# Optimization experiments

Hardware: AMD Instinct MI355X
Metric: run time of the kernel (lower is better)

Reference implementation:

```python
import jax, jax.numpy as jnp
import numpy as np

NUM_HEADS = 12


def setup_inputs() -> dict:
    key = jax.random.key(0)
    ks = jax.random.split(key, 5)
    B, S, D = 4, 2048, 768
    scale = 0.02
    return {
        "hidden_states": jax.random.normal(ks[0], (B, S, D), dtype=jnp.float32),
        "c_attn_w": jax.random.normal(ks[1], (D, 3 * D), dtype=jnp.float32) * scale,
        "c_attn_b": jax.random.normal(ks[2], (3 * D,), dtype=jnp.float32) * scale,
        "c_proj_w": jax.random.normal(ks[3], (D, D), dtype=jnp.float32) * scale,
        "c_proj_b": jax.random.normal(ks[4], (D,), dtype=jnp.float32) * scale,
    }


def reference(hidden_states, c_attn_w, c_attn_b, c_proj_w, c_proj_b):
    B, S, D = hidden_states.shape
    H = NUM_HEADS
    hd = D // H

    # fused QKV projection (HF Conv1D: x @ W + b, W is [in, out])
    qkv = hidden_states @ c_attn_w + c_attn_b  # [B, S, 3D]
    q, k, v = jnp.split(qkv, 3, axis=-1)

    def split_heads(t):
        return t.reshape(B, S, H, hd).transpose(0, 2, 1, 3)  # [B, H, S, hd]

    q, k, v = split_heads(q), split_heads(k), split_heads(v)

    # scaled dot-product scores (scale_attn_weights=True -> / sqrt(head_dim))
    scores = jnp.einsum("bhqd,bhkd->bhqk", q, k) / jnp.asarray(
        np.sqrt(hd), dtype=q.dtype
    )

    # causal mask: where(tril, scores, dtype_min) as in eager GPT2Attention
    causal = jnp.tril(jnp.ones((S, S), dtype=bool))
    mask_value = jnp.finfo(scores.dtype).min
    scores = jnp.where(causal[None, None, :, :], scores, mask_value)

    attn = jax.nn.softmax(scores, axis=-1)  # attn_dropout p=0 (eval)

    out = jnp.einsum("bhqk,bhkd->bhqd", attn, v)
    out = out.transpose(0, 2, 1, 3).reshape(B, S, D)  # merge heads

    # output projection (resid_dropout p=0)
    return out @ c_proj_w + c_proj_b
```

## Files before the change

kernel.cpp:

```cpp
#include <hip/hip_runtime.h>
#include <stdint.h>

typedef __attribute__((ext_vector_type(8))) short short8;
typedef __attribute__((ext_vector_type(4))) short short4v;
typedef __attribute__((ext_vector_type(8))) __bf16 bf16x8;
typedef __attribute__((ext_vector_type(4))) float f32x4;

#define SEQ 2048
#define DMODEL 768
#define NHEAD 12
#define HD 64
#define NBATCH 4

#define QSCALE 0.18033688011112042f

__device__ __forceinline__ float bf2f(unsigned short u) {
    return __uint_as_float(((unsigned int)u) << 16);
}
__device__ __forceinline__ unsigned short f2bf(float f) {
    unsigned int u = __float_as_uint(f);
    u += 0x7fffu + ((u >> 16) & 1u);
    return (unsigned short)(u >> 16);
}
__device__ __forceinline__ unsigned short f2bfn(float f) {
    union { __bf16 h; unsigned short u; } cv;
    cv.h = (__bf16)f;
    return cv.u;
}
__device__ __forceinline__ short8 cvt8(float4 a, float4 b) {
    short8 r;
    r[0] = (short)f2bf(a.x); r[1] = (short)f2bf(a.y);
    r[2] = (short)f2bf(a.z); r[3] = (short)f2bf(a.w);
    r[4] = (short)f2bf(b.x); r[5] = (short)f2bf(b.y);
    r[6] = (short)f2bf(b.z); r[7] = (short)f2bf(b.w);
    return r;
}
__device__ __forceinline__ f32x4 mfma16(short8 a, short8 b, f32x4 c) {
    return __builtin_amdgcn_mfma_f32_16x16x32_bf16(
        __builtin_bit_cast(bf16x8, a), __builtin_bit_cast(bf16x8, b), c, 0, 0, 0);
}
__device__ __forceinline__ f32x4 mfma16k16(short4v a, short4v b, f32x4 c) {
#if __has_builtin(__builtin_amdgcn_mfma_f32_16x16x16bf16_1k)
    return __builtin_amdgcn_mfma_f32_16x16x16bf16_1k(a, b, c, 0, 0, 0);
#else
    asm("v_mfma_f32_16x16x16_bf16 %0, %1, %2, %0" : "+v"(c) : "v"(a), "v"(b));
    return c;
#endif
}
__device__ __forceinline__ void gload16(const unsigned short* g, unsigned short* l) {
    __builtin_amdgcn_global_load_lds(
        (const __attribute__((address_space(1))) unsigned int*)g,
        (__attribute__((address_space(3))) unsigned int*)l, 16, 0, 0);
}

__global__ void detect_k(const unsigned short* x, const unsigned short* w1,
                         const unsigned short* b1, const unsigned short* w2,
                         const unsigned short* b2, int* flags) {
    const int w = threadIdx.x >> 6, l = threadIdx.x & 63;
    if (w >= 5) return;
    const unsigned short* ptrs[5] = {x, w1, b1, w2, b2};
    const unsigned short* p = ptrs[w];
    float mx = 0.f;
    for (int j = l; j < 1024; j += 64) {
        float v = fabsf(bf2f(p[j]));
        if (!(v <= 1e30f)) v = 1e31f;
        if (v > mx) mx = v;
    }
#pragma unroll
    for (int off = 1; off < 64; off <<= 1) mx = fmaxf(mx, __shfl_xor(mx, off, 64));
    if (l == 0) flags[w] = (mx > 1e3f) ? 1 : 0;
}

__global__ __launch_bounds__(256) void cvt_x(
    const float* __restrict__ Xf, const unsigned short* __restrict__ Xh,
    unsigned short* __restrict__ Xb, const int* __restrict__ flags, int n8) {
    int i = blockIdx.x * 256 + threadIdx.x;
    if (i >= n8) return;
    if (flags[0]) {
        float4 a = ((const float4*)Xf)[(size_t)i * 2];
        float4 b = ((const float4*)Xf)[(size_t)i * 2 + 1];
        *(short8*)&Xb[(size_t)i * 8] = cvt8(a, b);
    } else {
        ((uint4*)Xb)[i] = ((const uint4*)Xh)[i];
    }
}

__device__ __forceinline__ void wt_body(
    unsigned short (*tile)[65], const float* __restrict__ Wf,
    const unsigned short* __restrict__ Wh, unsigned short* __restrict__ Wt,
    int R, int C, bool f32, int bx, int by, int t) {

    const int c0 = bx * 64, r0 = by * 64;
    const int ri = t >> 2, cj = (t & 3) * 16;

    if (f32) {
#pragma unroll
        for (int u = 0; u < 4; u++) {
            float4 v = *(const float4*)&Wf[(size_t)(r0 + ri) * C + c0 + cj + u * 4];
            tile[ri][cj + u * 4 + 0] = f2bf(v.x);
            tile[ri][cj + u * 4 + 1] = f2bf(v.y);
            tile[ri][cj + u * 4 + 2] = f2bf(v.z);
            tile[ri][cj + u * 4 + 3] = f2bf(v.w);
        }
    } else {
        uint4 a = *(const uint4*)&Wh[(size_t)(r0 + ri) * C + c0 + cj];
        uint4 b = *(const uint4*)&Wh[(size_t)(r0 + ri) * C + c0 + cj + 8];
        *(uint4*)&tile[ri][cj] = a;
        *(uint4*)&tile[ri][cj + 8] = b;
    }
    __syncthreads();

    const int ci = t >> 2, rj = (t & 3) * 16;
    unsigned short tmp[16];
#pragma unroll
    for (int u = 0; u < 16; u++) tmp[u] = tile[rj + u][ci];
    *(uint4*)&Wt[(size_t)(c0 + ci) * R + r0 + rj]     = *(uint4*)&tmp[0];
    *(uint4*)&Wt[(size_t)(c0 + ci) * R + r0 + rj + 8] = *(uint4*)&tmp[8];
}

__global__ __launch_bounds__(256) void convert_wt_both(
    const float* __restrict__ Wf1, const unsigned short* __restrict__ Wh1,
    unsigned short* __restrict__ Wt1,
    const float* __restrict__ Wf2, const unsigned short* __restrict__ Wh2,
    unsigned short* __restrict__ Wt2, const int* __restrict__ flags) {

    __shared__ unsigned short tile[64][65];
    const int t = threadIdx.x;
    if (blockIdx.y < 12) {
        wt_body(tile, Wf1, Wh1, Wt1, 768, 2304, flags[1] != 0,
                (int)blockIdx.x, (int)blockIdx.y, t);
    } else {
        if (blockIdx.x >= 12) return;
        wt_body(tile, Wf2, Wh2, Wt2, 768, 768, flags[3] != 0,
                (int)blockIdx.x, (int)blockIdx.y - 12, t);
    }
}

#define GSTG(buf, s) do {                                                          \
    unsigned short* BsF_ = &Bs[buf][0][0];                                         \
    gload16(&Bp[(size_t)(ch0 >> 2) * K + (s) * 32 + (ch0 & 3) * 8],                \
            BsF_ + (size_t)(w * 2 + 0) * 512);                                     \
    gload16(&Bp[(size_t)(ch1 >> 2) * K + (s) * 32 + (ch1 & 3) * 8],                \
            BsF_ + (size_t)(w * 2 + 1) * 512);                                     \
    if (af32) {                                                                    \
        float4 f0_ = *(const float4*)&Afp[(size_t)arow * K + (s) * 32 + acol];     \
        float4 f1_ = *(const float4*)&Afp[(size_t)arow * K + (s) * 32 + acol + 4]; \
        float4 f2_ = *(const float4*)&Afp[(size_t)(arow + 64) * K + (s) * 32 + acol];     \
        float4 f3_ = *(const float4*)&Afp[(size_t)(arow + 64) * K + (s) * 32 + acol + 4]; \
        *(short8*)&As[buf][arow][acol]      = cvt8(f0_, f1_);                      \
        *(short8*)&As[buf][arow + 64][acol] = cvt8(f2_, f3_);                      \
    } else {                                                                       \
        unsigned short* AsF_ = &As[buf][0][0];                                     \
        gload16(&Ahp[(size_t)(ch0 >> 2) * K + (s) * 32 + (ch0 & 3) * 8],           \
                AsF_ + (size_t)(w * 2 + 0) * 512);                                 \
        gload16(&Ahp[(size_t)(ch1 >> 2) * K + (s) * 32 + (ch1 & 3) * 8],           \
                AsF_ + (size_t)(w * 2 + 1) * 512);                                 \
    }                                                                              \
} while (0)

#define GSYNC() do {                                                               \
    if (af32) asm volatile("s_waitcnt vmcnt(0) lgkmcnt(0)" ::: "memory");          \
    else      asm volatile("s_waitcnt vmcnt(0)" ::: "memory");                     \
    __builtin_amdgcn_s_barrier();                                                  \
} while (0)

__global__ __launch_bounds__(256, 4) void gemm_bt(
    const float* __restrict__ Af, const unsigned short* __restrict__ Ah,
    const unsigned short* __restrict__ Bt,
    const float* __restrict__ biasf, const unsigned short* __restrict__ biash,
    int K, int mode, const int* __restrict__ flags, int aFidx, int bFidx,
    unsigned short* __restrict__ out0, unsigned short* __restrict__ out1,
    unsigned short* __restrict__ out2, float* __restrict__ outf) {

    __shared__ __align__(16) unsigned short As[2][128][32];
    __shared__ __align__(16) unsigned short Bs[2][128][32];

    int bx = blockIdx.x, by = blockIdx.y;
    {
        const int nwg = (int)(gridDim.x * gridDim.y);
        if ((nwg & 7) == 0) {
            int bid = by * gridDim.x + bx;
            const int cpx = nwg >> 3;
            bid = (bid & 7) * cpx + (bid >> 3);
            bx = bid % gridDim.x;
            by = bid / gridDim.x;
        }
    }
    const int mBase = by * 128;
    const int nBase = bx * 128;
    const int t = threadIdx.x;
    const int w = t >> 6, l = t & 63, lr = l & 15, lk = l >> 4;
    const int wr = w >> 1, wc = w & 1;

    const bool af32 = (aFidx >= 0) && (flags[aFidx] != 0);
    const bool bf32 = flags[bFidx] != 0;

    f32x4 zero = {0.f, 0.f, 0.f, 0.f};
    f32x4 acc[4][4];
#pragma unroll
    for (int i = 0; i < 4; i++)
#pragma unroll
        for (int j = 0; j < 4; j++) acc[i][j] = zero;

    const int arow = t >> 2;
    const int acol = (t & 3) * 8;
    const float* Afp = Af + (size_t)mBase * K;
    const unsigned short* Ahp = Ah + (size_t)mBase * K;
    const unsigned short* Bp = Bt + (size_t)nBase * K;

    const int ch0 = (w * 2 + 0) * 64 + l;
    const int ch1 = (w * 2 + 1) * 64 + l;

    const int nsteps = K >> 5;

    GSTG(0, 0);
    GSYNC();

    int cur = 0;
    for (int s = 0; s < nsteps; ++s) {
        if (s + 1 < nsteps) GSTG(cur ^ 1, s + 1);

        short8 a[4], b[4];
#pragma unroll
        for (int i = 0; i < 4; i++)
            a[i] = *(const short8*)&As[cur][wr * 64 + i * 16 + lr][lk * 8];
#pragma unroll
        for (int j = 0; j < 4; j++)
            b[j] = *(const short8*)&Bs[cur][wc * 64 + j * 16 + lr][lk * 8];
#pragma unroll
        for (int i = 0; i < 4; i++)
#pragma unroll
            for (int j = 0; j < 4; j++) acc[i][j] = mfma16(a[i], b[j], acc[i][j]);

        if (s + 1 < nsteps) GSYNC();
        cur ^= 1;
    }

#pragma unroll
    for (int j = 0; j < 4; j++) {
        int col = nBase + wc * 64 + j * 16 + lr;
        float bv = bf32 ? biasf[col] : bf2f(biash[col]);
        if (mode == 0 && col >= 1536) {
            int c2 = col - 1536;
            int h = c2 >> 6, d = c2 & 63;
#pragma unroll
            for (int i = 0; i < 4; i++) {
                int row0 = mBase + wr * 64 + i * 16 + lk * 4;
                int bb = row0 >> 11, s0 = row0 & 2047;
                short4v hv4;
#pragma unroll
                for (int r = 0; r < 4; r++) hv4[r] = (short)f2bf(acc[i][j][r] + bv);
                *(short4v*)&out2[(((size_t)(bb * NHEAD + h)) * HD + d) * SEQ + s0] = hv4;
            }
        } else {
#pragma unroll
            for (int i = 0; i < 4; i++) {
                int row0 = mBase + wr * 64 + i * 16 + lk * 4;
#pragma unroll
                for (int r = 0; r < 4; r++) {
                    int row = row0 + r;
                    float fv = acc[i][j][r] + bv;
                    if (mode == 0) {
                        int bb = row >> 11;
                        int s  = row & 2047;
                        if (col < 768) {
                            int h = col >> 6, d = col & 63;
                            out0[(((size_t)(bb * NHEAD + h)) * SEQ + s) * HD + d] =
                                f2bf(fv * QSCALE);
                        } else {
                            int c2 = col - 768;
                            int h = c2 >> 6, d = c2 & 63;
                            out1[(((size_t)(bb * NHEAD + h)) * SEQ + s) * HD + d] =
                                f2bf(fv);
                        }
                    } else {
                        outf[(size_t)row * DMODEL + col] = fv;
                    }
                }
            }
        }
    }
}

#define STAGE(buf, tile) do {                                                  \
    _Pragma("unroll")                                                          \
    for (int q_ = 0; q_ < 2; ++q_) {                                           \
        const int c_ = w * 128 + q_ * 64 + l;                                  \
        const int row_ = c_ >> 3;                                              \
        const int ch_ = (c_ & 7) ^ (row_ & 7);                                 \
        gload16(&Kp[(size_t)((tile) * 64 + row_) * HD + ch_ * 8],              \
                &Ks[buf][(w * 128 + q_ * 64) * 8]);                            \
        gload16(&Vp[(size_t)row_ * SEQ + (tile) * 64 + ch_ * 8],               \
                &Vs[buf][(w * 128 + q_ * 64) * 8]);                            \
    }                                                                          \
} while (0)

__global__ __launch_bounds__(256, 3) void flash_attn(
    const unsigned short* __restrict__ Q, const unsigned short* __restrict__ Km,
    const unsigned short* __restrict__ Vt, unsigned short* __restrict__ Oatt) {

    const int h  = blockIdx.x;
    const int px = (7 * blockIdx.y + blockIdx.x + blockIdx.z) & 15;
    const int b  = blockIdx.z;
    const int bh = b * NHEAD + h;
    const int qtA = 31 - px;
    const int qtB = px;
    const int t = threadIdx.x, w = t >> 6, l = t & 63, lr = l & 15, lk = l >> 4;
    const int qbA = qtA * 64 + w * 16;
    const int qbB = qtB * 64 + w * 16;

    const unsigned short* Qp = Q + (size_t)bh * SEQ * HD;
    const unsigned short* Kp = Km + (size_t)bh * SEQ * HD;
    const unsigned short* Vp = Vt + (size_t)bh * HD * SEQ;

    __shared__ __align__(16) unsigned short Ks[3][4096];
    __shared__ __align__(16) unsigned short Vs[3][4096];

    short8 qA0 = *(const short8*)&Qp[(size_t)(qbA + lr) * HD + lk * 8];
    short8 qA1 = *(const short8*)&Qp[(size_t)(qbA + lr) * HD + 32 + lk * 8];
    short8 qB0 = *(const short8*)&Qp[(size_t)(qbB + lr) * HD + lk * 8];
    short8 qB1 = *(const short8*)&Qp[(size_t)(qbB + lr) * HD + 32 + lk * 8];

    f32x4 zero = {0.f, 0.f, 0.f, 0.f};
    f32x4 oA[4], oB[4];
    float lsumA = 0.f, lsumB = 0.f;
#pragma unroll
    for (int dt = 0; dt < 4; dt++) { oA[dt] = zero; oB[dt] = zero; }

    STAGE(0, 0);
    STAGE(1, 1);
    asm volatile("s_waitcnt vmcnt(4)" ::: "memory");
    __builtin_amdgcn_s_barrier();

    int cur = 0;
    for (int kt = 0; kt <= qtA; ++kt) {
        const bool pf = (kt + 2 <= qtA);
        if (pf) {
            const int st = (cur == 0) ? 2 : cur - 1;
            STAGE(st, kt + 2);
        }
        const bool doB = (kt <= qtB);

        f32x4 s0[4], s1[4];
        __builtin_amdgcn_s_setprio(1);
#pragma unroll
        for (int ct = 0; ct < 4; ct++) {
            const int row = ct * 16 + lr, sw = row & 7;
            short8 k0 = *(const short8*)&Ks[cur][(row * 8 + (lk ^ sw)) * 8];
            short8 k1 = *(const short8*)&Ks[cur][(row * 8 + ((4 | lk) ^ sw)) * 8];
            s0[ct] = mfma16(k0, qA0, zero);
            s0[ct] = mfma16(k1, qA1, s0[ct]);
            if (doB) {
                s1[ct] = mfma16(k0, qB0, zero);
                s1[ct] = mfma16(k1, qB1, s1[ct]);
            }
        }
        __builtin_amdgcn_s_setprio(0);

        short4v vf[4][4];
#pragma unroll
        for (int dt = 0; dt < 4; dt++) {
            const int row = dt * 16 + lr;
            const int sw = row & 7;
#pragma unroll
            for (int ct = 0; ct < 4; ct++) {
                const int g = 2 * ct + (lk >> 1);
                const int hh = lk & 1;
                vf[dt][ct] = *(const short4v*)&Vs[cur][(row * 8 + (g ^ sw)) * 8 + hh * 4];
            }
        }

        short4v paA[4];
        {
            float p[4][4];
#pragma unroll
            for (int ct = 0; ct < 4; ct++)
#pragma unroll
                for (int r = 0; r < 4; r++) p[ct][r] = exp2f(s0[ct][r]);
            if (kt == qtA) {
                const int qrow = qbA + lr;
#pragma unroll
                for (int ct = 0; ct < 4; ct++)
#pragma unroll
                    for (int r = 0; r < 4; r++) {
                        const int key = kt * 64 + ct * 16 + lk * 4 + r;
                        if (key > qrow) p[ct][r] = 0.0f;
                    }
            }
#pragma unroll
            for (int ct = 0; ct < 4; ct++)
                lsumA += (p[ct][0] + p[ct][1]) + (p[ct][2] + p[ct][3]);
#pragma unroll
            for (int ct = 0; ct < 4; ct++) {
                short4v pk;
#pragma unroll
                for (int r = 0; r < 4; r++) pk[r] = (short)f2bfn(p[ct][r]);
                paA[ct] = pk;
            }
        }
        __builtin_amdgcn_s_setprio(1);
#pragma unroll
        for (int dt = 0; dt < 4; dt++)
#pragma unroll
            for (int ct = 0; ct < 4; ct++)
                oA[dt] = mfma16k16(paA[ct], vf[dt][ct], oA[dt]);
        __builtin_amdgcn_s_setprio(0);

        if (doB) {
            short4v paB[4];
            float p[4][4];
#pragma unroll
            for (int ct = 0; ct < 4; ct++)
#pragma unroll
                for (int r = 0; r < 4; r++) p[ct][r] = exp2f(s1[ct][r]);
            if (kt == qtB) {
                const int qrow = qbB + lr;
#pragma unroll
                for (int ct = 0; ct < 4; ct++)
#pragma unroll
                    for (int r = 0; r < 4; r++) {
                        const int key = kt * 64 + ct * 16 + lk * 4 + r;
                        if (key > qrow) p[ct][r] = 0.0f;
                    }
            }
#pragma unroll
            for (int ct = 0; ct < 4; ct++)
                lsumB += (p[ct][0] + p[ct][1]) + (p[ct][2] + p[ct][3]);
#pragma unroll
            for (int ct = 0; ct < 4; ct++) {
                short4v pk;
#pragma unroll
                for (int r = 0; r < 4; r++) pk[r] = (short)f2bfn(p[ct][r]);
                paB[ct] = pk;
            }
            __builtin_amdgcn_s_setprio(1);
#pragma unroll
            for (int dt = 0; dt < 4; dt++)
#pragma unroll
                for (int ct = 0; ct < 4; ct++)
                    oB[dt] = mfma16k16(paB[ct], vf[dt][ct], oB[dt]);
            __builtin_amdgcn_s_setprio(0);
        }

        if (kt < qtA) {
            if (pf) asm volatile("s_waitcnt vmcnt(4)" ::: "memory");
            else    asm volatile("s_waitcnt vmcnt(0)" ::: "memory");
            __builtin_amdgcn_s_barrier();
        }
        cur = (cur == 2) ? 0 : cur + 1;
    }

    lsumA += __shfl_xor(lsumA, 16, 64);
    lsumA += __shfl_xor(lsumA, 32, 64);
    lsumB += __shfl_xor(lsumB, 16, 64);
    lsumB += __shfl_xor(lsumB, 32, 64);

#pragma unroll
    for (int r = 0; r < 4; r++) {
        const float invA = 1.0f / __shfl(lsumA, lk * 4 + r, 64);
        const float invB = 1.0f / __shfl(lsumB, lk * 4 + r, 64);
        const int rowA = qbA + lk * 4 + r;
        const int rowB = qbB + lk * 4 + r;
#pragma unroll
        for (int dt = 0; dt < 4; dt++) {
            Oatt[((size_t)(b * SEQ) + rowA) * DMODEL + h * HD + dt * 16 + lr] =
                f2bfn(oA[dt][r] * invA);
            Oatt[((size_t)(b * SEQ) + rowB) * DMODEL + h * HD + dt * 16 + lr] =
                f2bfn(oB[dt][r] * invB);
        }
    }
}

extern "C" void kernel_launch(void* const* d_in, const int* in_sizes, int n_in,
                              void* d_out, int out_size, void* d_ws, size_t ws_size,
                              hipStream_t stream) {
    const void *X = d_in[0], *W1 = d_in[1], *b1 = d_in[2], *W2 = d_in[3], *b2 = d_in[4];
    for (int i = 0; i < n_in; i++) {
        switch (in_sizes[i]) {
            case NBATCH * SEQ * DMODEL: X  = d_in[i]; break;
            case DMODEL * 3 * DMODEL:   W1 = d_in[i]; break;
            case 3 * DMODEL:            b1 = d_in[i]; break;
            case DMODEL * DMODEL:       W2 = d_in[i]; break;
            case DMODEL:                b2 = d_in[i]; break;
        }
    }
    float* out = (float*)d_out;

    int* flags = (int*)d_ws;
    unsigned short* base = (unsigned short*)d_ws + 64;
    unsigned short* Wt1 = base;
    unsigned short* Wt2 = Wt1 + (size_t)2304 * 768;

    const size_t headElems = (size_t)NHEAD * SEQ * HD;
    const size_t xElems = (size_t)NBATCH * SEQ * DMODEL;
    const size_t fixedElems = 64 + (size_t)2304 * 768 + (size_t)768 * 768;
    const size_t mergedNeed = (fixedElems + xElems + 4 * NBATCH * headElems) * 2 + 1024;
    const bool merged = ws_size >= mergedNeed;

    detect_k<<<1, 320, 0, stream>>>(
        (const unsigned short*)X, (const unsigned short*)W1,
        (const unsigned short*)b1, (const unsigned short*)W2,
        (const unsigned short*)b2, flags);

    convert_wt_both<<<dim3(36, 24), 256, 0, stream>>>(
        (const float*)W1, (const unsigned short*)W1, Wt1,
        (const float*)W2, (const unsigned short*)W2, Wt2, flags);

    if (merged) {
        unsigned short* Xb  = Wt2 + (size_t)768 * 768;
        unsigned short* Qw  = Xb + xElems;
        unsigned short* Kw  = Qw + (size_t)NBATCH * headElems;
        unsigned short* Vtw = Kw + (size_t)NBATCH * headElems;
        unsigned short* Aw  = Vtw + (size_t)NBATCH * headElems;

        cvt_x<<<(int)((xElems / 8 + 255) / 256), 256, 0, stream>>>(
            (const float*)X, (const unsigned short*)X, Xb, flags, (int)(xElems / 8));

        gemm_bt<<<dim3(2304 / 128, NBATCH * SEQ / 128), 256, 0, stream>>>(
            nullptr, Xb, Wt1,
            (const float*)b1, (const unsigned short*)b1,
            DMODEL, 0, flags, -1, 2, Qw, Kw, Vtw, nullptr);

        flash_attn<<<dim3(NHEAD, 16, NBATCH), 256, 0, stream>>>(Qw, Kw, Vtw, Aw);

        gemm_bt<<<dim3(768 / 128, NBATCH * SEQ / 128), 256, 0, stream>>>(
            nullptr, Aw, Wt2,
            (const float*)b2, (const unsigned short*)b2,
            DMODEL, 1, flags, -1, 4, nullptr, nullptr, nullptr, out);
    } else {
        unsigned short* Qw  = Wt2 + (size_t)768 * 768;
        unsigned short* Kw  = Qw + headElems;
        unsigned short* Vtw = Kw + headElems;
        unsigned short* Aw  = Vtw + headElems;
        for (int batch = 0; batch < NBATCH; ++batch) {
            const size_t xoff = (size_t)batch * SEQ * DMODEL;

            gemm_bt<<<dim3(2304 / 128, SEQ / 128), 256, 0, stream>>>(
                (const float*)X + xoff, (const unsigned short*)X + xoff, Wt1,
                (const float*)b1, (const unsigned short*)b1,
                DMODEL, 0, flags, 0, 2, Qw, Kw, Vtw, nullptr);

            flash_attn<<<dim3(NHEAD, 16, 1), 256, 0, stream>>>(Qw, Kw, Vtw, Aw);

            gemm_bt<<<dim3(768 / 128, SEQ / 128), 256, 0, stream>>>(
                nullptr, Aw, Wt2,
                (const float*)b2, (const unsigned short*)b2,
                DMODEL, 1, flags, -1, 4, nullptr, nullptr, nullptr, out + xoff);
        }
    }
}
```

Baseline: 236.8 us.

## Triple-buffer GEMM staging and unroll attention loop by three with constant buffer offsets

The GEMM kernel moves from double to triple buffered LDS tiles, prefetching two steps ahead with a partial vmcnt wait instead of draining all loads. Its launch-bounds occupancy hint drops from 4 to 3 to fit the larger shared memory. The flash attention loop is unrolled three times so the rotating buffer index becomes a compile-time constant, and the swizzled LDS offsets are precomputed outside the loop. This aims to hide global load latency and remove per-iteration address math, at the cost of more LDS, lower occupancy in the GEMM and larger code.

Result: slower. 305.9 us (+29.2%).

```diff
diff --git a/kernel.cpp b/kernel.cpp
--- a/kernel.cpp
+++ b/kernel.cpp
@@ -158,13 +158,7 @@
     }                                                                              \
 } while (0)
 
-#define GSYNC() do {                                                               \
-    if (af32) asm volatile("s_waitcnt vmcnt(0) lgkmcnt(0)" ::: "memory");          \
-    else      asm volatile("s_waitcnt vmcnt(0)" ::: "memory");                     \
-    __builtin_amdgcn_s_barrier();                                                  \
-} while (0)
-
-__global__ __launch_bounds__(256, 4) void gemm_bt(
+__global__ __launch_bounds__(256, 3) void gemm_bt(
     const float* __restrict__ Af, const unsigned short* __restrict__ Ah,
     const unsigned short* __restrict__ Bt,
     const float* __restrict__ biasf, const unsigned short* __restrict__ biash,
@@ -172,8 +166,8 @@
     unsigned short* __restrict__ out0, unsigned short* __restrict__ out1,
     unsigned short* __restrict__ out2, float* __restrict__ outf) {
 
-    __shared__ __align__(16) unsigned short As[2][128][32];
-    __shared__ __align__(16) unsigned short Bs[2][128][32];
+    __shared__ __align__(16) unsigned short As[3][128][32];
+    __shared__ __align__(16) unsigned short Bs[3][128][32];
 
     int bx = blockIdx.x, by = blockIdx.y;
     {
@@ -214,11 +208,18 @@
     const int nsteps = K >> 5;
 
     GSTG(0, 0);
-    GSYNC();
+    GSTG(1, 1);
+    if (af32) { asm volatile("s_waitcnt vmcnt(0) lgkmcnt(0)" ::: "memory"); }
+    else      { asm volatile("s_waitcnt vmcnt(4)" ::: "memory"); }
+    __builtin_amdgcn_s_barrier();
 
     int cur = 0;
     for (int s = 0; s < nsteps; ++s) {
-        if (s + 1 < nsteps) GSTG(cur ^ 1, s + 1);
+        const bool pf = (s + 2 < nsteps);
+        if (pf) {
+            const int st = (cur == 0) ? 2 : cur - 1;
+            GSTG(st, s + 2);
+        }
 
         short8 a[4], b[4];
 #pragma unroll
@@ -232,8 +233,13 @@
 #pragma unroll
             for (int j = 0; j < 4; j++) acc[i][j] = mfma16(a[i], b[j], acc[i][j]);
 
-        if (s + 1 < nsteps) GSYNC();
-        cur ^= 1;
+        if (s + 1 < nsteps) {
+            if (af32)    { asm volatile("s_waitcnt vmcnt(0) lgkmcnt(0)" ::: "memory"); }
+            else if (pf) { asm volatile("s_waitcnt vmcnt(4)" ::: "memory"); }
+            else         { asm volatile("s_waitcnt vmcnt(0)" ::: "memory"); }
+            __builtin_amdgcn_s_barrier();
+        }
+        cur = (cur == 2) ? 0 : cur + 1;
     }
 
 #pragma unroll
@@ -295,6 +301,113 @@
     }                                                                          \
 } while (0)
 
+#define FBODY(CUR) do {                                                        \
+    const bool pf = (kt + 2 <= qtA);                                           \
+    if (pf) STAGE((((CUR) + 2) % 3), kt + 2);                                  \
+    const bool doB = (kt <= qtB);                                              \
+    f32x4 s0[4], s1[4];                                                        \
+    __builtin_amdgcn_s_setprio(1);                                             \
+    _Pragma("unroll")                                                          \
+    for (int ct = 0; ct < 4; ct++) {                                           \
+        short8 k0 = *(const short8*)&KsF[(CUR) * 4096 + ct * 1024 + k0off];    \
+        short8 k1 = *(const short8*)&KsF[(CUR) * 4096 + ct * 1024 + k1off];    \
+        s0[ct] = mfma16(k0, qA0, zero);                                        \
+        s0[ct] = mfma16(k1, qA1, s0[ct]);                                      \
+        if (doB) {                                                             \
+            s1[ct] = mfma16(k0, qB0, zero);                                    \
+            s1[ct] = mfma16(k1, qB1, s1[ct]);                                  \
+        }                                                                      \
+    }                                                                          \
+    __builtin_amdgcn_s_setprio(0);                                             \
+    short4v vf0[4], vf1[4], vf2[4], vf3[4];                                    \
+    _Pragma("unroll")                                                          \
+    for (int dt = 0; dt < 4; dt++) {                                           \
+        vf0[dt] = *(const short4v*)&VsF[(CUR) * 4096 + dt * 1024 + voff0];     \
+        vf1[dt] = *(const short4v*)&VsF[(CUR) * 4096 + dt * 1024 + voff1];     \
+        vf2[dt] = *(const short4v*)&VsF[(CUR) * 4096 + dt * 1024 + voff2];     \
+        vf3[dt] = *(const short4v*)&VsF[(CUR) * 4096 + dt * 1024 + voff3];     \
+    }                                                                          \
+    short4v paA[4];                                                            \
+    {                                                                          \
+        float p[4][4];                                                         \
+        _Pragma("unroll")                                                      \
+        for (int ct = 0; ct < 4; ct++)                                         \
+            _Pragma("unroll")                                                  \
+            for (int r = 0; r < 4; r++) p[ct][r] = exp2f(s0[ct][r]);           \
+        if (kt == qtA) {                                                       \
+            const int qrow = qbA + lr;                                         \
+            _Pragma("unroll")                                                  \
+            for (int ct = 0; ct < 4; ct++)                                     \
+                _Pragma("unroll")                                              \
+                for (int r = 0; r < 4; r++) {                                  \
+                    const int key = kt * 64 + ct * 16 + lk * 4 + r;            \
+                    if (key > qrow) p[ct][r] = 0.0f;                           \
+                }                                                              \
+        }                                                                      \
+        _Pragma("unroll")                                                      \
+        for (int ct = 0; ct < 4; ct++)                                         \
+            lsumA += (p[ct][0] + p[ct][1]) + (p[ct][2] + p[ct][3]);            \
+        _Pragma("unroll")                                                      \
+        for (int ct = 0; ct < 4; ct++) {                                       \
+            short4v pk;                                                        \
+            _Pragma("unroll")                                                  \
+            for (int r = 0; r < 4; r++) pk[r] = (short)f2bfn(p[ct][r]);        \
+            paA[ct] = pk;                                                      \
+        }                                                                      \
+    }                                                                          \
+    __builtin_amdgcn_s_setprio(1);                                             \
+    _Pragma("unroll")                                                          \
+    for (int dt = 0; dt < 4; dt++) {                                           \
+        oA[dt] = mfma16k16(paA[0], vf0[dt], oA[dt]);                           \
+        oA[dt] = mfma16k16(paA[1], vf1[dt], oA[dt]);                           \
+        oA[dt] = mfma16k16(paA[2], vf2[dt], oA[dt]);                           \
+        oA[dt] = mfma16k16(paA[3], vf3[dt], oA[dt]);                           \
+    }                                                                          \
+    __builtin_amdgcn_s_setprio(0);                                             \
+    if (doB) {                                                                 \
+        short4v paB[4];                                                        \
+        float p[4][4];                                                         \
+        _Pragma("unroll")                                                      \
+        for (int ct = 0; ct < 4; ct++)                                         \
+            _Pragma("unroll")                                                  \
+            for (int r = 0; r < 4; r++) p[ct][r] = exp2f(s1[ct][r]);           \
+        if (kt == qtB) {                                                       \
+            const int qrow = qbB + lr;                                         \
+            _Pragma("unroll")                                                  \
+            for (int ct = 0; ct < 4; ct++)                                     \
+                _Pragma("unroll")                                              \
+                for (int r = 0; r < 4; r++) {                                  \
+                    const int key = kt * 64 + ct * 16 + lk * 4 + r;            \
+                    if (key > qrow) p[ct][r] = 0.0f;                           \
+                }                                                              \
+        }                                                                      \
+        _Pragma("unroll")                                                      \
+        for (int ct = 0; ct < 4; ct++)                                         \
+            lsumB += (p[ct][0] + p[ct][1]) + (p[ct][2] + p[ct][3]);            \
+        _Pragma("unroll")                                                      \
+        for (int ct = 0; ct < 4; ct++) {                                       \
+            short4v pk;                                                        \
+            _Pragma("unroll")                                                  \
+            for (int r = 0; r < 4; r++) pk[r] = (short)f2bfn(p[ct][r]);        \
+            paB[ct] = pk;                                                      \
+        }                                                                      \
+        __builtin_amdgcn_s_setprio(1);                                         \
+        _Pragma("unroll")                                                      \
+        for (int dt = 0; dt < 4; dt++) {                                       \
+            oB[dt] = mfma16k16(paB[0], vf0[dt], oB[dt]);                       \
+            oB[dt] = mfma16k16(paB[1], vf1[dt], oB[dt]);                       \
+            oB[dt] = mfma16k16(paB[2], vf2[dt], oB[dt]);                       \
+            oB[dt] = mfma16k16(paB[3], vf3[dt], oB[dt]);                       \
+        }                                                                      \
+        __builtin_amdgcn_s_setprio(0);                                         \
+    }                                                                          \
+    if (kt < qtA) {                                                            \
+        if (pf) asm volatile("s_waitcnt vmcnt(4)" ::: "memory");               \
+        else    asm volatile("s_waitcnt vmcnt(0)" ::: "memory");               \
+        __builtin_amdgcn_s_barrier();                                          \
+    }                                                                          \
+} while (0)
+
 __global__ __launch_bounds__(256, 3) void flash_attn(
     const unsigned short* __restrict__ Q, const unsigned short* __restrict__ Km,
     const unsigned short* __restrict__ Vt, unsigned short* __restrict__ Oatt) {
@@ -315,6 +428,8 @@
 
     __shared__ __align__(16) unsigned short Ks[3][4096];
     __shared__ __align__(16) unsigned short Vs[3][4096];
+    const unsigned short* KsF = &Ks[0][0];
+    const unsigned short* VsF = &Vs[0][0];
 
     short8 qA0 = *(const short8*)&Qp[(size_t)(qbA + lr) * HD + lk * 8];
     short8 qA1 = *(const short8*)&Qp[(size_t)(qbA + lr) * HD + 32 + lk * 8];
@@ -327,128 +442,29 @@
 #pragma unroll
     for (int dt = 0; dt < 4; dt++) { oA[dt] = zero; oB[dt] = zero; }
 
+    const int sw = lr & 7;
+    const int k0off = lr * 64 + ((lk ^ sw) * 8);
+    const int k1off = lr * 64 + ((((4 | lk)) ^ sw) * 8);
+    const int q2 = lk >> 1, hh2 = (lk & 1) * 4;
+    const int voff0 = lr * 64 + (((0 + q2) ^ sw) * 8) + hh2;
+    const int voff1 = lr * 64 + (((2 + q2) ^ sw) * 8) + hh2;
+    const int voff2 = lr * 64 + (((4 + q2) ^ sw) * 8) + hh2;
+    const int voff3 = lr * 64 + (((6 + q2) ^ sw) * 8) + hh2;
+
     STAGE(0, 0);
     STAGE(1, 1);
     asm volatile("s_waitcnt vmcnt(4)" ::: "memory");
     __builtin_amdgcn_s_barrier();
 
-    int cur = 0;
-    for (int kt = 0; kt <= qtA; ++kt) {
-        const bool pf = (kt + 2 <= qtA);
-        if (pf) {
-            const int st = (cur == 0) ? 2 : cur - 1;
-            STAGE(st, kt + 2);
-        }
-        const bool doB = (kt <= qtB);
-
-        f32x4 s0[4], s1[4];
-        __builtin_amdgcn_s_setprio(1);
-#pragma unroll
-        for (int ct = 0; ct < 4; ct++) {
-            const int row = ct * 16 + lr, sw = row & 7;
-            short8 k0 = *(const short8*)&Ks[cur][(row * 8 + (lk ^ sw)) * 8];
-            short8 k1 = *(const short8*)&Ks[cur][(row * 8 + ((4 | lk) ^ sw)) * 8];
-            s0[ct] = mfma16(k0, qA0, zero);
-            s0[ct] = mfma16(k1, qA1, s0[ct]);
-            if (doB) {
-                s1[ct] = mfma16(k0, qB0, zero);
-                s1[ct] = mfma16(k1, qB1, s1[ct]);
-            }
-        }
-        __builtin_amdgcn_s_setprio(0);
-
-        short4v vf[4][4];
-#pragma unroll
-        for (int dt = 0; dt < 4; dt++) {
-            const int row = dt * 16 + lr;
-            const int sw = row & 7;
-#pragma unroll
-            for (int ct = 0; ct < 4; ct++) {
-                const int g = 2 * ct + (lk >> 1);
-                const int hh = lk & 1;
-                vf[dt][ct] = *(const short4v*)&Vs[cur][(row * 8 + (g ^ sw)) * 8 + hh * 4];
-            }
-        }
-
-        short4v paA[4];
-        {
-            float p[4][4];
-#pragma unroll
-            for (int ct = 0; ct < 4; ct++)
-#pragma unroll
-                for (int r = 0; r < 4; r++) p[ct][r] = exp2f(s0[ct][r]);
-            if (kt == qtA) {
-                const int qrow = qbA + lr;
-#pragma unroll
-                for (int ct = 0; ct < 4; ct++)
-#pragma unroll
-                    for (int r = 0; r < 4; r++) {
-                        const int key = kt * 64 + ct * 16 + lk * 4 + r;
-                        if (key > qrow) p[ct][r] = 0.0f;
-                    }
-            }
-#pragma unroll
-            for (int ct = 0; ct < 4; ct++)
-                lsumA += (p[ct][0] + p[ct][1]) + (p[ct][2] + p[ct][3]);
-#pragma unroll
-            for (int ct = 0; ct < 4; ct++) {
-                short4v pk;
-#pragma unroll
-                for (int r = 0; r < 4; r++) pk[r] = (short)f2bfn(p[ct][r]);
-                paA[ct] = pk;
-            }
-        }
-        __builtin_amdgcn_s_setprio(1);
-#pragma unroll
-        for (int dt = 0; dt < 4; dt++)
-#pragma unroll
-            for (int ct = 0; ct < 4; ct++)
-                oA[dt] = mfma16k16(paA[ct], vf[dt][ct], oA[dt]);
-        __builtin_amdgcn_s_setprio(0);
-
-        if (doB) {
-            short4v paB[4];
-            float p[4][4];
-#pragma unroll
-            for (int ct = 0; ct < 4; ct++)
-#pragma unroll
-                for (int r = 0; r < 4; r++) p[ct][r] = exp2f(s1[ct][r]);
-            if (kt == qtB) {
-                const int qrow = qbB + lr;
-#pragma unroll
-                for (int ct = 0; ct < 4; ct++)
-#pragma unroll
-                    for (int r = 0; r < 4; r++) {
-                        const int key = kt * 64 + ct * 16 + lk * 4 + r;
-                        if (key > qrow) p[ct][r] = 0.0f;
-                    }
-            }
-#pragma unroll
-            for (int ct = 0; ct < 4; ct++)
-                lsumB += (p[ct][0] + p[ct][1]) + (p[ct][2] + p[ct][3]);
-#pragma unroll
-            for (int ct = 0; ct < 4; ct++) {
-                short4v pk;
-#pragma unroll
-                for (int r = 0; r < 4; r++) pk[r] = (short)f2bfn(p[ct][r]);
-                paB[ct] = pk;
-            }
-            __builtin_amdgcn_s_setprio(1);
-#pragma unroll
-            for (int dt = 0; dt < 4; dt++)
-#pragma unroll
-                for (int ct = 0; ct < 4; ct++)
-                    oB[dt] = mfma16k16(paB[ct], vf[dt][ct], oB[dt]);
-            __builtin_amdgcn_s_setprio(0);
-        }
-
-        if (kt < qtA) {
-            if (pf) asm volatile("s_waitcnt vmcnt(4)" ::: "memory");
-            else    asm volatile("s_waitcnt vmcnt(0)" ::: "memory");
-            __builtin_amdgcn_s_barrier();
-        }
-        cur = (cur == 2) ? 0 : cur + 1;
-    }
+    const int NT = qtA + 1;
+    int kt = 0;
+    while (kt + 3 <= NT) {
+        FBODY(0); kt++;
+        FBODY(1); kt++;
+        FBODY(2); kt++;
+    }
+    if (kt < NT) { FBODY(0); kt++; }
+    if (kt < NT) { FBODY(1); kt++; }
 
     lsumA += __shfl_xor(lsumA, 16, 64);
     lsumA += __shfl_xor(lsumA, 32, 64);
```
